# Optimization experiments

Measured on AMD Instinct MI355X. Metric: run time of the kernel, lower is better.

## Reference

```python
import jax, jax.numpy as jnp
import numpy as np

WINDOW_SIZE = 11
PAD = WINDOW_SIZE // 2


def _box_filter(x):
    """Depthwise uniform box filter, separable: two 1D convs with 1/W weights.

    x: [N, C, H, W] float. Zero padding of PAD on each side (matches torch
    F.conv2d(padding=PAD) with the outer-product uniform window).
    """
    c = x.shape[1]
    w = jnp.full((c, 1, WINDOW_SIZE, 1), 1.0 / WINDOW_SIZE, dtype=x.dtype)
    # vertical pass
    y = jax.lax.conv_general_dilated(
        x, w, window_strides=(1, 1), padding=((PAD, PAD), (0, 0)),
        dimension_numbers=('NCHW', 'OIHW', 'NCHW'), feature_group_count=c)
    # horizontal pass
    w2 = jnp.transpose(w, (0, 1, 3, 2))  # [C,1,1,WINDOW_SIZE]
    y = jax.lax.conv_general_dilated(
        y, w2, window_strides=(1, 1), padding=((0, 0), (PAD, PAD)),
        dimension_numbers=('NCHW', 'OIHW', 'NCHW'), feature_group_count=c)
    return y


def _ssim_loss(img1, img2):
    C1 = 0.01 ** 2
    C2 = 0.03 ** 2
    mu1 = _box_filter(img1)
    mu2 = _box_filter(img2)
    mu1_sq = mu1 * mu1
    mu2_sq = mu2 * mu2
    mu1_mu2 = mu1 * mu2
    sigma1_sq = _box_filter(img1 * img1) - mu1_sq
    sigma2_sq = _box_filter(img2 * img2) - mu2_sq
    sigma12 = _box_filter(img1 * img2) - mu1_mu2
    ssim_map = ((2 * mu1_mu2 + C1) * (2 * sigma12 + C2)) / (
        (mu1_sq + mu2_sq + C1) * (sigma1_sq + sigma2_sq + C2))
    return 1.0 - jnp.mean(ssim_map)


def setup_inputs() -> dict:
    key = jax.random.key(0)
    k1, k2 = jax.random.split(key)
    shape = (16, 3, 512, 512)
    img1 = jax.random.uniform(k1, shape, dtype=jnp.float32)
    img2 = jax.random.uniform(k2, shape, dtype=jnp.float32)
    return {"img1": img1, "img2": img2}


def reference(img1, img2):
    return _ssim_loss(img1, img2)
```

## Files before the change

kernel.cpp:

```cpp
#include <hip/hip_runtime.h>
#include <math.h>


typedef __fp16 half2_t __attribute__((ext_vector_type(2)));
typedef __fp16 half4_t __attribute__((ext_vector_type(4)));

constexpr int WIN  = 11;
constexpr int OTW  = 116;
constexpr int INW  = 128;
constexpr int OTH  = 32;
constexpr int VP   = 131;
constexpr int SEGR = 8;
constexpr int SEGI = SEGR + WIN - 1;
constexpr int GPW  = 15;
constexpr int H = 512, W = 512;
constexpr int NPLANES = 16 * 3;
constexpr int GRIDX = (W + OTW - 1) / OTW;
constexpr long long NPIX = (long long)NPLANES * H * W;

__device__ __forceinline__ half4_t pack4(float a, float b, float c, float d) {
    const half2_t lo = __builtin_amdgcn_cvt_pkrtz(a, b);
    const half2_t hi = __builtin_amdgcn_cvt_pkrtz(c, d);
    half4_t r;
    r[0] = lo[0]; r[1] = lo[1]; r[2] = hi[0]; r[3] = hi[1];
    return r;
}

__device__ __forceinline__ float ssim_px(float ws, float wd, float wss, float wdd) {
    const float C1 = 1e-4f;
    const float C2 = 9e-4f;
    const float k1 = 1.0f / 121.0f;
    const float ka = 0.25f * k1 * k1;
    const float kb = 0.5f  * k1 * k1;
    const float kc = 0.25f * k1;
    const float kd = 0.5f  * k1;
    const float ws2 = ws * ws, wd2 = wd * wd;
    const float mu12 = ka * (ws2 - wd2);
    const float musq = kb * (ws2 + wd2);
    const float q12  = kc * (wss - wdd);
    const float qsum = kd * (wss + wdd);
    const float sig12  = q12 - mu12;
    const float sigsum = qsum - musq;
    const float num = fmaf(2.0f, mu12, C1) * fmaf(2.0f, sig12, C2);
    const float den = (musq + C1) * (sigsum + C2);
    return num * __builtin_amdgcn_rcpf(den);
}

__device__ __forceinline__ float ssim_h(half2_t alo, half2_t ahi) {
    return ssim_px((float)alo[0], (float)alo[1], (float)ahi[0], (float)ahi[1]);
}

template<bool XE, bool YE>
__device__ __forceinline__ void vpass(const float* __restrict__ ca,
                                      const float* __restrict__ cb,
                                      int gy0, bool xok0, bool xok1,
                                      int vrow0, int lane, half4_t (*V)[VP]) {
    float sh0[WIN], dh0[WIN], sh1[WIN], dh1[WIN];
    float ss0 = 0.f, sd0 = 0.f, sss0 = 0.f, sdd0 = 0.f;
    float ss1 = 0.f, sd1 = 0.f, sss1 = 0.f, sdd1 = 0.f;
#pragma unroll
    for (int r = 0; r < SEGI; ++r) {
        float a0, a1, b0, b1;
        if (YE) {
            const int gy = gy0 + r;
            a0 = a1 = b0 = b1 = 0.f;
            if ((unsigned)gy < (unsigned)H) {
                const float2 va = *(const float2*)(ca + (size_t)gy * W);
                const float2 vb = *(const float2*)(cb + (size_t)gy * W);
                a0 = va.x; a1 = va.y; b0 = vb.x; b1 = vb.y;
            }
        } else {
            const float2 va = *(const float2*)(ca + (size_t)(gy0 + r) * W);
            const float2 vb = *(const float2*)(cb + (size_t)(gy0 + r) * W);
            a0 = va.x; a1 = va.y; b0 = vb.x; b1 = vb.y;
        }
        if (XE) {
            a0 = xok0 ? a0 : 0.f;  b0 = xok0 ? b0 : 0.f;
            a1 = xok1 ? a1 : 0.f;  b1 = xok1 ? b1 : 0.f;
        }
        const int i = r % WIN;
        const float s0 = a0 + b0, d0 = a0 - b0;
        const float s1 = a1 + b1, d1 = a1 - b1;
        ss0 += s0; sd0 += d0; sss0 = fmaf(s0, s0, sss0); sdd0 = fmaf(d0, d0, sdd0);
        ss1 += s1; sd1 += d1; sss1 = fmaf(s1, s1, sss1); sdd1 = fmaf(d1, d1, sdd1);
        if (r >= WIN) {
            const float so0 = sh0[i], do0 = dh0[i];
            const float so1 = sh1[i], do1 = dh1[i];
            ss0 -= so0; sd0 -= do0; sss0 = fmaf(-so0, so0, sss0); sdd0 = fmaf(-do0, do0, sdd0);
            ss1 -= so1; sd1 -= do1; sss1 = fmaf(-so1, so1, sss1); sdd1 = fmaf(-do1, do1, sdd1);
        }
        sh0[i] = s0; dh0[i] = d0; sh1[i] = s1; dh1[i] = d1;
        if (r >= WIN - 1) {
            const int vr = vrow0 + r - (WIN - 1);
            V[vr][2 * lane]     = pack4(ss0, sd0, sss0, sdd0);
            V[vr][2 * lane + 1] = pack4(ss1, sd1, sss1, sdd1);
        }
    }
}

__global__ __launch_bounds__(256, 4)
void ssim_tile_kernel(const float* __restrict__ img1,
                      const float* __restrict__ img2,
                      float* __restrict__ partials) {
    __shared__ half4_t V[OTH][VP];
    __shared__ float wsum[4];

    const int tid  = threadIdx.x;
    const int wave = tid >> 6;
    const int lane = tid & 63;
    const int tx0 = blockIdx.x * OTW;
    const int ty0 = blockIdx.y * OTH;
    const int plane = blockIdx.z;
    const float* __restrict__ pa = img1 + (size_t)plane * H * W;
    const float* __restrict__ pb = img2 + (size_t)plane * H * W;

    {
        const int gxl = tx0 - 6 + 2 * lane;
        const bool xok0 = (unsigned)gxl < (unsigned)W;
        const bool xok1 = (unsigned)(gxl + 1) < (unsigned)W;
        const int gc = min(max(gxl, 0), W - 2);
        const int gy0 = ty0 + wave * SEGR - (WIN / 2);
        const int vrow0 = wave * SEGR;
        const bool xe = (blockIdx.x == 0) || (blockIdx.x == GRIDX - 1);
        const bool ye = (gy0 < 0) || (gy0 + SEGI > H);
        const float* __restrict__ ca = pa + gc;
        const float* __restrict__ cb = pb + gc;
        if (!xe) {
            if (!ye) vpass<false, false>(ca, cb, gy0, xok0, xok1, vrow0, lane, V);
            else     vpass<false, true >(ca, cb, gy0, xok0, xok1, vrow0, lane, V);
        } else {
            if (!ye) vpass<true, false>(ca, cb, gy0, xok0, xok1, vrow0, lane, V);
            else     vpass<true, true >(ca, cb, gy0, xok0, xok1, vrow0, lane, V);
        }
    }
    if (tid < 96) {
        const int row = tid / 3, c = 128 + tid % 3;
        half4_t z; z[0] = (__fp16)0; z[1] = (__fp16)0; z[2] = (__fp16)0; z[3] = (__fp16)0;
        V[row][c] = z;
    }
    __syncthreads();

    const int row = tid & 31;
    const int x0  = (tid >> 5) * GPW;
    const int gxb = tx0 + x0;
    half2_t alo = {(__fp16)0, (__fp16)0};
    half2_t ahi = alo;
#pragma unroll
    for (int r = 0; r < WIN; ++r) {
        const half4_t v = V[row][x0 + 1 + r];
        const half2_t vl = {v[0], v[1]};
        const half2_t vh = {v[2], v[3]};
        alo += vl; ahi += vh;
    }
    float local = 0.0f;
    if (gxb < W)
        local = ssim_h(alo, ahi);
#pragma unroll
    for (int k = 1; k < GPW; ++k) {
        const half4_t vn = V[row][x0 + k + WIN];
        const half4_t vo = V[row][x0 + k];
        const half2_t dl = {(__fp16)(vn[0] - vo[0]), (__fp16)(vn[1] - vo[1])};
        const half2_t dh = {(__fp16)(vn[2] - vo[2]), (__fp16)(vn[3] - vo[3])};
        alo += dl; ahi += dh;
        if (x0 + k < OTW && gxb + k < W)
            local += ssim_h(alo, ahi);
    }

    for (int off = 32; off > 0; off >>= 1)
        local += __shfl_down(local, off);
    if ((tid & 63) == 0) wsum[wave] = local;
    __syncthreads();
    if (tid == 0) {
        const int bid = (blockIdx.z * gridDim.y + blockIdx.y) * gridDim.x + blockIdx.x;
        partials[bid] = wsum[0] + wsum[1] + wsum[2] + wsum[3];
    }
}

__global__ __launch_bounds__(1024)
void ssim_reduce_kernel(const float4* __restrict__ partials4, int n4,
                        float* __restrict__ out) {
    double s = 0.0;
    for (int i = threadIdx.x; i < n4; i += 1024) {
        const float4 p = partials4[i];
        s += (double)p.x + (double)p.y + (double)p.z + (double)p.w;
    }
    for (int off = 32; off > 0; off >>= 1)
        s += __shfl_down(s, off);
    __shared__ double wsum[16];
    if ((threadIdx.x & 63) == 0) wsum[threadIdx.x >> 6] = s;
    __syncthreads();
    if (threadIdx.x == 0) {
        double total = 0.0;
        for (int w = 0; w < 16; ++w) total += wsum[w];
        out[0] = (float)(1.0 - total / (double)NPIX);
    }
}

extern "C" void kernel_launch(void* const* d_in, const int* in_sizes, int n_in,
                              void* d_out, int out_size, void* d_ws, size_t ws_size,
                              hipStream_t stream) {
    const float* img1 = (const float*)d_in[0];
    const float* img2 = (const float*)d_in[1];
    float* out = (float*)d_out;
    float* partials = (float*)d_ws;

    dim3 grid(GRIDX, H / OTH, NPLANES);
    dim3 block(256);
    ssim_tile_kernel<<<grid, block, 0, stream>>>(img1, img2, partials);

    const int nblocks = GRIDX * (H / OTH) * NPLANES;
    ssim_reduce_kernel<<<1, 1024, 0, stream>>>((const float4*)partials,
                                               nblocks / 4, out);
}
```

Before: 38.60 us.

## Double tile height, remap horizontal pass to one row per lane, simplify SSIM math

Raises the output tile height from 32 to 64 rows with 16-row vertical segments per wave. Each lane now handles one full row of the horizontal pass over 29 columns, so the halo padding and its zero-fill are gone and the shared array is narrower. The horizontal pass uses packed half4 adds and is templated to drop bounds checks on non-edge blocks, and the per-pixel SSIM formula is refactored to use fewer multiplies. Launch bounds drop to 2 blocks per CU because of the larger LDS tile, which lowers occupancy, and longer fp16 running sums may accumulate more rounding error.

Measured after the change: 56.57 us. 46.6% more time.

```diff
diff --git a/kernel.cpp b/kernel.cpp
--- a/kernel.cpp
+++ b/kernel.cpp
@@ -7,12 +7,11 @@
 
 constexpr int WIN  = 11;
 constexpr int OTW  = 116;
-constexpr int INW  = 128;
-constexpr int OTH  = 32;
-constexpr int VP   = 131;
-constexpr int SEGR = 8;
+constexpr int OTH  = 64;
+constexpr int VP   = 127;
+constexpr int SEGR = 16;
 constexpr int SEGI = SEGR + WIN - 1;
-constexpr int GPW  = 15;
+constexpr int GPW  = 29;
 constexpr int H = 512, W = 512;
 constexpr int NPLANES = 16 * 3;
 constexpr int GRIDX = (W + OTW - 1) / OTW;
@@ -30,24 +29,23 @@
     const float C1 = 1e-4f;
     const float C2 = 9e-4f;
     const float k1 = 1.0f / 121.0f;
-    const float ka = 0.25f * k1 * k1;
-    const float kb = 0.5f  * k1 * k1;
-    const float kc = 0.25f * k1;
-    const float kd = 0.5f  * k1;
-    const float ws2 = ws * ws, wd2 = wd * wd;
-    const float mu12 = ka * (ws2 - wd2);
-    const float musq = kb * (ws2 + wd2);
-    const float q12  = kc * (wss - wdd);
-    const float qsum = kd * (wss + wdd);
-    const float sig12  = q12 - mu12;
-    const float sigsum = qsum - musq;
-    const float num = fmaf(2.0f, mu12, C1) * fmaf(2.0f, sig12, C2);
-    const float den = (musq + C1) * (sigsum + C2);
+    const float c2a = 0.5f * k1 * k1;
+    const float c2c = 0.5f * k1;
+    const float P = (c2a * ws) * ws;
+    const float Q = (c2a * wd) * wd;
+    const float U = c2c * wss;
+    const float T = c2c * wdd;
+    const float r1 = P - Q;
+    const float p1 = P + Q;
+    const float t1 = U - T;
+    const float u1 = U + T;
+    const float num = (r1 + C1) * (t1 - r1 + C2);
+    const float den = (p1 + C1) * (u1 - p1 + C2);
     return num * __builtin_amdgcn_rcpf(den);
 }
 
-__device__ __forceinline__ float ssim_h(half2_t alo, half2_t ahi) {
-    return ssim_px((float)alo[0], (float)alo[1], (float)ahi[0], (float)ahi[1]);
+__device__ __forceinline__ float ssim_h(half4_t acc) {
+    return ssim_px((float)acc[0], (float)acc[1], (float)acc[2], (float)acc[3]);
 }
 
 template<bool XE, bool YE>
@@ -58,6 +56,7 @@
     float sh0[WIN], dh0[WIN], sh1[WIN], dh1[WIN];
     float ss0 = 0.f, sd0 = 0.f, sss0 = 0.f, sdd0 = 0.f;
     float ss1 = 0.f, sd1 = 0.f, sss1 = 0.f, sdd1 = 0.f;
+    const bool wr1 = (lane != 63);
 #pragma unroll
     for (int r = 0; r < SEGI; ++r) {
         float a0, a1, b0, b1;
@@ -92,13 +91,33 @@
         sh0[i] = s0; dh0[i] = d0; sh1[i] = s1; dh1[i] = d1;
         if (r >= WIN - 1) {
             const int vr = vrow0 + r - (WIN - 1);
-            V[vr][2 * lane]     = pack4(ss0, sd0, sss0, sdd0);
-            V[vr][2 * lane + 1] = pack4(ss1, sd1, sss1, sdd1);
-        }
-    }
-}
-
-__global__ __launch_bounds__(256, 4)
+            V[vr][2 * lane] = pack4(ss0, sd0, sss0, sdd0);
+            if (wr1)
+                V[vr][2 * lane + 1] = pack4(ss1, sd1, sss1, sdd1);
+        }
+    }
+}
+
+template<bool CHK>
+__device__ __forceinline__ float hpass(const half4_t (*V)[VP], int row, int x0,
+                                       int gxb) {
+    half4_t acc = {(__fp16)0, (__fp16)0, (__fp16)0, (__fp16)0};
+#pragma unroll
+    for (int r = 0; r < WIN; ++r)
+        acc += V[row][x0 + 1 + r];
+    float local = 0.0f;
+    if (!CHK || gxb < W)
+        local = ssim_h(acc);
+#pragma unroll
+    for (int k = 1; k < GPW; ++k) {
+        acc += V[row][x0 + k + WIN] - V[row][x0 + k];
+        if (!CHK || gxb + k < W)
+            local += ssim_h(acc);
+    }
+    return local;
+}
+
+__global__ __launch_bounds__(256, 2)
 void ssim_tile_kernel(const float* __restrict__ img1,
                       const float* __restrict__ img2,
                       float* __restrict__ partials) {
@@ -133,42 +152,20 @@
             else     vpass<true, true >(ca, cb, gy0, xok0, xok1, vrow0, lane, V);
         }
     }
-    if (tid < 96) {
-        const int row = tid / 3, c = 128 + tid % 3;
-        half4_t z; z[0] = (__fp16)0; z[1] = (__fp16)0; z[2] = (__fp16)0; z[3] = (__fp16)0;
-        V[row][c] = z;
-    }
     __syncthreads();
 
-    const int row = tid & 31;
-    const int x0  = (tid >> 5) * GPW;
+    const int row = lane;
+    const int x0  = wave * GPW;
     const int gxb = tx0 + x0;
-    half2_t alo = {(__fp16)0, (__fp16)0};
-    half2_t ahi = alo;
-#pragma unroll
-    for (int r = 0; r < WIN; ++r) {
-        const half4_t v = V[row][x0 + 1 + r];
-        const half2_t vl = {v[0], v[1]};
-        const half2_t vh = {v[2], v[3]};
-        alo += vl; ahi += vh;
-    }
-    float local = 0.0f;
-    if (gxb < W)
-        local = ssim_h(alo, ahi);
-#pragma unroll
-    for (int k = 1; k < GPW; ++k) {
-        const half4_t vn = V[row][x0 + k + WIN];
-        const half4_t vo = V[row][x0 + k];
-        const half2_t dl = {(__fp16)(vn[0] - vo[0]), (__fp16)(vn[1] - vo[1])};
-        const half2_t dh = {(__fp16)(vn[2] - vo[2]), (__fp16)(vn[3] - vo[3])};
-        alo += dl; ahi += dh;
-        if (x0 + k < OTW && gxb + k < W)
-            local += ssim_h(alo, ahi);
-    }
+    float local;
+    if (blockIdx.x != GRIDX - 1)
+        local = hpass<false>(V, row, x0, gxb);
+    else
+        local = hpass<true >(V, row, x0, gxb);
 
     for (int off = 32; off > 0; off >>= 1)
         local += __shfl_down(local, off);
-    if ((tid & 63) == 0) wsum[wave] = local;
+    if (lane == 0) wsum[wave] = local;
     __syncthreads();
     if (tid == 0) {
         const int bid = (blockIdx.z * gridDim.y + blockIdx.y) * gridDim.x + blockIdx.x;
```
